# Performance work log

Hardware: AMD Instinct MI355X
Metric: run time of the kernel (lower is better)

The kernel has to match this reference:

```python
import jax, jax.numpy as jnp
import numpy as np

N = 100_000      # nodes
E = 2_500_000    # edges (nnz), avg degree 25
D_IN = 32
D_OUT = 32


def setup_inputs() -> dict:
    key = jax.random.key(0)
    k1, k2, k3, k4 = jax.random.split(key, 4)
    X = jax.random.normal(k1, (N, D_IN), dtype=jnp.float32)
    # CSR row offsets: sorted, anchored at 0 and E
    rp = jnp.sort(jax.random.randint(k2, (N + 1,), 0, E, dtype=jnp.int32))
    rp = rp.at[0].set(0).at[-1].set(E)
    ci = jax.random.randint(k3, (E,), 0, N, dtype=jnp.int32)
    W = (jax.random.normal(k4, (D_IN, D_OUT), dtype=jnp.float32)
         * (1.0 / np.sqrt(D_OUT)).astype(np.float32))
    dummy = jnp.zeros((1,), dtype=jnp.int32)
    return {
        "X": X,
        "weights": W,
        "row_pointers": rp,
        "column_index": ci,
        "blockPartition": dummy,
        "edgeToColumn": dummy,
        "edgeToRow": dummy,
        "hybrid_type": dummy,
        "row_nzr": dummy,
        "col_nzr": dummy,
    }


def reference(X, weights, row_pointers, column_index, blockPartition,
              edgeToColumn, edgeToRow, hybrid_type, row_nzr, col_nzr):
    # Fused GIN: X_prime = A @ X (CSR neighbor sum), then X_prime @ W.
    # Recover per-edge destination row from CSR offsets: row r owns edges
    # in [row_pointers[r], row_pointers[r+1]).
    edge_ids = jnp.arange(E, dtype=row_pointers.dtype)
    row = jnp.searchsorted(row_pointers, edge_ids, side="right") - 1  # [E]
    gathered = X[column_index]                       # [E, D_IN] (irregular gather)
    X_prime = jax.ops.segment_sum(gathered, row, num_segments=N)  # [N, D_IN]
    return X_prime @ weights                          # [N, D_OUT]
```

## Files before the change

kernel.cpp:

```cpp
#include <hip/hip_runtime.h>

#define D 32

__global__ __launch_bounds__(256, 8)
void xw_kernel(const float* __restrict__ X, const float* __restrict__ W,
               float* __restrict__ Y, int n) {
    const int lane = threadIdx.x & 63;
    const int j    = lane & 31;
    const int wid  = blockIdx.x * (blockDim.x >> 6) + (threadIdx.x >> 6);
    const int nw   = gridDim.x * (blockDim.x >> 6);

    float w[D];
    #pragma unroll
    for (int d = 0; d < D; ++d) w[d] = W[d * D + j];

    for (int r = wid; r <= n; r += nw) {
        float o0 = 0.f, o1 = 0.f;
        if (r < n) {
            const float* xr =
                X + (size_t)(unsigned)__builtin_amdgcn_readfirstlane(r) * D;
            #pragma unroll
            for (int d = 0; d < D; d += 2) {
                o0 = fmaf(xr[d],     w[d],     o0);
                o1 = fmaf(xr[d + 1], w[d + 1], o1);
            }
        }
        if (lane < 32) Y[(size_t)r * D + j] = o0 + o1;
    }
}

template <int K>
__device__ __forceinline__ void gather_acc(const float* __restrict__ Y,
                                           int myci, int base, int g, int s,
                                           float4& acc) {
    float4 x[K];
    #pragma unroll
    for (int it = 0; it < K; ++it) {
        int c = __shfl(myci, (base + it) * 8 + g, 64);
        x[it] = ((const float4*)(Y + (size_t)(unsigned)c * D))[s];
    }
    #pragma unroll
    for (int it = 0; it < K; ++it) {
        acc.x += x[it].x; acc.y += x[it].y;
        acc.z += x[it].z; acc.w += x[it].w;
    }
}

__device__ __forceinline__ void ladder(const float* __restrict__ Y, int myci,
                                       int nv, int g, int s, float4& acc) {
    switch ((nv + 7) >> 3) {
        case 1: gather_acc<1>(Y, myci, 0, g, s, acc); break;
        case 2: gather_acc<2>(Y, myci, 0, g, s, acc); break;
        case 3: gather_acc<3>(Y, myci, 0, g, s, acc); break;
        case 4: gather_acc<4>(Y, myci, 0, g, s, acc); break;
        case 5: gather_acc<4>(Y, myci, 0, g, s, acc);
                gather_acc<1>(Y, myci, 4, g, s, acc); break;
        case 6: gather_acc<4>(Y, myci, 0, g, s, acc);
                gather_acc<2>(Y, myci, 4, g, s, acc); break;
        case 7: gather_acc<4>(Y, myci, 0, g, s, acc);
                gather_acc<3>(Y, myci, 4, g, s, acc); break;
        default: gather_acc<4>(Y, myci, 0, g, s, acc);
                 gather_acc<4>(Y, myci, 4, g, s, acc); break;
    }
}

__global__ __launch_bounds__(256, 8)
void agg_kernel(const float* __restrict__ Y, const int* __restrict__ rp,
                const int* __restrict__ ci, float* __restrict__ out, int n) {
    const int lane = threadIdx.x & 63;
    const int g  = lane >> 3;
    const int s  = lane & 7;
    const int zr = n;

    const int wid = (blockIdx.x * blockDim.x + threadIdx.x) >> 6;
    const int nw  = (gridDim.x * blockDim.x) >> 6;

    int r = __builtin_amdgcn_readfirstlane(wid);
    if (r >= n) return;

    int start = rp[r];
    int end   = rp[r + 1];
    {
        int nv0 = end - start; nv0 = nv0 > 64 ? 64 : nv0;
        start = start;
    }
    int nv0 = end - start; nv0 = nv0 > 64 ? 64 : nv0;
    int myci = (lane < nv0) ? ci[start + lane] : zr;

    while (true) {
        const int deg = end - start;
        const int rn  = r + nw;
        const bool has_next = rn < n;

        int nstart = 0, nend = 0, next_ci = zr;
        if (has_next) {
            nstart = rp[rn];
            nend   = rp[rn + 1];
            int nnv = nend - nstart; nnv = nnv > 64 ? 64 : nnv;
            next_ci = (lane < nnv) ? ci[nstart + lane] : zr;
        }

        float4 acc = make_float4(0.f, 0.f, 0.f, 0.f);
        if (deg > 0) {
            int nv = deg > 64 ? 64 : deg;
            ladder(Y, myci, nv, g, s, acc);
            for (int cb = 64; cb < deg; cb += 64) {
                int rem = deg - cb;
                int nv2 = rem > 64 ? 64 : rem;
                int c2  = (lane < nv2) ? ci[start + cb + lane] : zr;
                ladder(Y, c2, nv2, g, s, acc);
            }
        }

        #pragma unroll
        for (int off = 8; off < 64; off <<= 1) {
            acc.x += __shfl_xor(acc.x, off, 64);
            acc.y += __shfl_xor(acc.y, off, 64);
            acc.z += __shfl_xor(acc.z, off, 64);
            acc.w += __shfl_xor(acc.w, off, 64);
        }
        if (lane < 8) ((float4*)(out + (size_t)r * D))[s] = acc;

        if (!has_next) break;
        r = rn; start = nstart; end = nend; myci = next_ci;
    }
}

__global__ __launch_bounds__(256, 4)
void gin_fused(const float* __restrict__ X,
               const float* __restrict__ W,
               const int* __restrict__ rp,
               const int* __restrict__ ci,
               float* __restrict__ out,
               int n) {
    __shared__ float Wl[D * D];

    int tid = threadIdx.x;
    {
        const float4* Wv = (const float4*)W;
        float4* Wlv = (float4*)Wl;
        Wlv[tid] = Wv[tid];
    }
    __syncthreads();

    int wave = tid >> 6;
    int lane = tid & 63;
    int row = blockIdx.x * 4 + wave;
    if (row >= n) return;

    int start = rp[row];
    int deg   = rp[row + 1] - start;

    int g = lane >> 3;
    int s = lane & 7;

    float4 acc = make_float4(0.f, 0.f, 0.f, 0.f);

    for (int cb = 0; cb < deg; cb += 64) {
        int rem = deg - cb;
        int nv  = rem < 64 ? rem : 64;
        int myci = (lane < nv) ? ci[start + cb + lane] : 0;
        {
            float4 x[4]; float m[4];
            #pragma unroll
            for (int it = 0; it < 4; ++it) {
                int l = it * 8 + g;
                int c = __shfl(myci, l, 64);
                m[it] = (l < rem) ? 1.f : 0.f;
                x[it] = ((const float4*)(X + (size_t)c * D))[s];
            }
            #pragma unroll
            for (int it = 0; it < 4; ++it) {
                acc.x = fmaf(m[it], x[it].x, acc.x);
                acc.y = fmaf(m[it], x[it].y, acc.y);
                acc.z = fmaf(m[it], x[it].z, acc.z);
                acc.w = fmaf(m[it], x[it].w, acc.w);
            }
        }
        if (rem > 32) {
            float4 x[4]; float m[4];
            #pragma unroll
            for (int it = 0; it < 4; ++it) {
                int l = (it + 4) * 8 + g;
                int c = __shfl(myci, l, 64);
                m[it] = (l < rem) ? 1.f : 0.f;
                x[it] = ((const float4*)(X + (size_t)c * D))[s];
            }
            #pragma unroll
            for (int it = 0; it < 4; ++it) {
                acc.x = fmaf(m[it], x[it].x, acc.x);
                acc.y = fmaf(m[it], x[it].y, acc.y);
                acc.z = fmaf(m[it], x[it].z, acc.z);
                acc.w = fmaf(m[it], x[it].w, acc.w);
            }
        }
    }

    #pragma unroll
    for (int off = 8; off < 64; off <<= 1) {
        acc.x += __shfl_xor(acc.x, off, 64);
        acc.y += __shfl_xor(acc.y, off, 64);
        acc.z += __shfl_xor(acc.z, off, 64);
        acc.w += __shfl_xor(acc.w, off, 64);
    }

    int j = lane & 31;
    float o = 0.f;
    #pragma unroll
    for (int sg = 0; sg < 8; ++sg) {
        float ax = __shfl(acc.x, sg, 64);
        float ay = __shfl(acc.y, sg, 64);
        float az = __shfl(acc.z, sg, 64);
        float aw = __shfl(acc.w, sg, 64);
        int d = 4 * sg;
        o = fmaf(ax, Wl[(d    ) * D + j], o);
        o = fmaf(ay, Wl[(d + 1) * D + j], o);
        o = fmaf(az, Wl[(d + 2) * D + j], o);
        o = fmaf(aw, Wl[(d + 3) * D + j], o);
    }
    if (lane < 32) out[(size_t)row * D + j] = o;
}

extern "C" void kernel_launch(void* const* d_in, const int* in_sizes, int n_in,
                              void* d_out, int out_size, void* d_ws, size_t ws_size,
                              hipStream_t stream) {
    const float* X  = (const float*)d_in[0];
    const float* W  = (const float*)d_in[1];
    const int*   rp = (const int*)d_in[2];
    const int*   ci = (const int*)d_in[3];
    float* out = (float*)d_out;

    int n = in_sizes[2] - 1;
    size_t ybytes = (size_t)(n + 1) * D * sizeof(float);

    if (ws_size >= ybytes) {
        float* Y = (float*)d_ws;
        hipLaunchKernelGGL(xw_kernel, dim3(1024), dim3(256), 0, stream,
                           X, W, Y, n);
        int nwaves = (n + 3) / 4;
        int blocks = nwaves < 2048 ? nwaves : 2048;
        hipLaunchKernelGGL(agg_kernel, dim3(blocks), dim3(256), 0, stream,
                           Y, rp, ci, out, n);
    } else {
        hipLaunchKernelGGL(gin_fused, dim3((n + 3) / 4), dim3(256), 0, stream,
                           X, W, rp, ci, out, n);
    }
}
```

Before: 132.9 us.

## Store intermediate XW in fp16 and gather 16 edges per pass

The intermediate Y = X·W is now written as fp16, which halves the bytes the random neighbour gather in the aggregation kernel must fetch. Each lane now loads 8 halves, so 16 edges are handled per pass and the shuffle reduction and output store are reshaped to match. The xw kernel also processes two rows per wave using float4 loads, and its grid is doubled. The cost is reduced precision in the intermediate values, which may push results past the accuracy tolerance.

```diff
diff --git a/kernel.cpp b/kernel.cpp
--- a/kernel.cpp
+++ b/kernel.cpp
@@ -1,75 +1,74 @@
 #include <hip/hip_runtime.h>
 
 #define D 32
+
+typedef _Float16 half8 __attribute__((ext_vector_type(8)));
 
 __global__ __launch_bounds__(256, 8)
 void xw_kernel(const float* __restrict__ X, const float* __restrict__ W,
-               float* __restrict__ Y, int n) {
+               _Float16* __restrict__ Y16, int n) {
     const int lane = threadIdx.x & 63;
     const int j    = lane & 31;
-    const int wid  = blockIdx.x * (blockDim.x >> 6) + (threadIdx.x >> 6);
-    const int nw   = gridDim.x * (blockDim.x >> 6);
+    const int h    = lane >> 5;
+    const int wid  = (blockIdx.x * blockDim.x + threadIdx.x) >> 6;
+    const int nw   = (gridDim.x * blockDim.x) >> 6;
 
     float w[D];
     #pragma unroll
     for (int d = 0; d < D; ++d) w[d] = W[d * D + j];
 
-    for (int r = wid; r <= n; r += nw) {
-        float o0 = 0.f, o1 = 0.f;
+    for (int r0 = 2 * wid; r0 <= n; r0 += 2 * nw) {
+        const int r = r0 + h;
+        float o = 0.f;
         if (r < n) {
-            const float* xr =
-                X + (size_t)(unsigned)__builtin_amdgcn_readfirstlane(r) * D;
-            #pragma unroll
-            for (int d = 0; d < D; d += 2) {
-                o0 = fmaf(xr[d],     w[d],     o0);
-                o1 = fmaf(xr[d + 1], w[d + 1], o1);
-            }
-        }
-        if (lane < 32) Y[(size_t)r * D + j] = o0 + o1;
+            const float4* xr = (const float4*)(X + (size_t)r * D);
+            #pragma unroll
+            for (int k = 0; k < 8; ++k) {
+                float4 xv = xr[k];
+                o = fmaf(xv.x, w[4 * k    ], o);
+                o = fmaf(xv.y, w[4 * k + 1], o);
+                o = fmaf(xv.z, w[4 * k + 2], o);
+                o = fmaf(xv.w, w[4 * k + 3], o);
+            }
+        }
+        if (r <= n) Y16[(size_t)r * D + j] = (_Float16)o;
     }
 }
 
 template <int K>
-__device__ __forceinline__ void gather_acc(const float* __restrict__ Y,
-                                           int myci, int base, int g, int s,
-                                           float4& acc) {
-    float4 x[K];
+__device__ __forceinline__ void gather16(const _Float16* __restrict__ Y16,
+                                         int myci, int base, int g, int s,
+                                         float* acc) {
+    half8 x[K];
     #pragma unroll
     for (int it = 0; it < K; ++it) {
-        int c = __shfl(myci, (base + it) * 8 + g, 64);
-        x[it] = ((const float4*)(Y + (size_t)(unsigned)c * D))[s];
+        int c = __shfl(myci, (base + it) * 16 + g, 64);
+        x[it] = ((const half8*)(Y16 + (size_t)(unsigned)c * D))[s];
     }
     #pragma unroll
     for (int it = 0; it < K; ++it) {
-        acc.x += x[it].x; acc.y += x[it].y;
-        acc.z += x[it].z; acc.w += x[it].w;
-    }
-}
-
-__device__ __forceinline__ void ladder(const float* __restrict__ Y, int myci,
-                                       int nv, int g, int s, float4& acc) {
-    switch ((nv + 7) >> 3) {
-        case 1: gather_acc<1>(Y, myci, 0, g, s, acc); break;
-        case 2: gather_acc<2>(Y, myci, 0, g, s, acc); break;
-        case 3: gather_acc<3>(Y, myci, 0, g, s, acc); break;
-        case 4: gather_acc<4>(Y, myci, 0, g, s, acc); break;
-        case 5: gather_acc<4>(Y, myci, 0, g, s, acc);
-                gather_acc<1>(Y, myci, 4, g, s, acc); break;
-        case 6: gather_acc<4>(Y, myci, 0, g, s, acc);
-                gather_acc<2>(Y, myci, 4, g, s, acc); break;
-        case 7: gather_acc<4>(Y, myci, 0, g, s, acc);
-                gather_acc<3>(Y, myci, 4, g, s, acc); break;
-        default: gather_acc<4>(Y, myci, 0, g, s, acc);
-                 gather_acc<4>(Y, myci, 4, g, s, acc); break;
+        #pragma unroll
+        for (int e = 0; e < 8; ++e) acc[e] += (float)x[it][e];
+    }
+}
+
+__device__ __forceinline__ void ladder16(const _Float16* __restrict__ Y16,
+                                         int myci, int nv, int g, int s,
+                                         float* acc) {
+    switch ((nv + 15) >> 4) {
+        case 1:  gather16<1>(Y16, myci, 0, g, s, acc); break;
+        case 2:  gather16<2>(Y16, myci, 0, g, s, acc); break;
+        case 3:  gather16<3>(Y16, myci, 0, g, s, acc); break;
+        default: gather16<4>(Y16, myci, 0, g, s, acc); break;
     }
 }
 
 __global__ __launch_bounds__(256, 8)
-void agg_kernel(const float* __restrict__ Y, const int* __restrict__ rp,
+void agg_kernel(const _Float16* __restrict__ Y16, const int* __restrict__ rp,
                 const int* __restrict__ ci, float* __restrict__ out, int n) {
     const int lane = threadIdx.x & 63;
-    const int g  = lane >> 3;
-    const int s  = lane & 7;
+    const int g  = lane >> 2;
+    const int s  = lane & 3;
     const int zr = n;
 
     const int wid = (blockIdx.x * blockDim.x + threadIdx.x) >> 6;
@@ -80,12 +79,8 @@
 
     int start = rp[r];
     int end   = rp[r + 1];
-    {
-        int nv0 = end - start; nv0 = nv0 > 64 ? 64 : nv0;
-        start = start;
-    }
-    int nv0 = end - start; nv0 = nv0 > 64 ? 64 : nv0;
-    int myci = (lane < nv0) ? ci[start + lane] : zr;
+    int nv0   = end - start; nv0 = nv0 > 64 ? 64 : nv0;
+    int myci  = (lane < nv0) ? ci[start + lane] : zr;
 
     while (true) {
         const int deg = end - start;
@@ -100,26 +95,28 @@
             next_ci = (lane < nnv) ? ci[nstart + lane] : zr;
         }
 
-        float4 acc = make_float4(0.f, 0.f, 0.f, 0.f);
+        float acc[8] = {0.f, 0.f, 0.f, 0.f, 0.f, 0.f, 0.f, 0.f};
         if (deg > 0) {
             int nv = deg > 64 ? 64 : deg;
-            ladder(Y, myci, nv, g, s, acc);
+            ladder16(Y16, myci, nv, g, s, acc);
             for (int cb = 64; cb < deg; cb += 64) {
                 int rem = deg - cb;
                 int nv2 = rem > 64 ? 64 : rem;
                 int c2  = (lane < nv2) ? ci[start + cb + lane] : zr;
-                ladder(Y, c2, nv2, g, s, acc);
+                ladder16(Y16, c2, nv2, g, s, acc);
             }
         }
 
         #pragma unroll
-        for (int off = 8; off < 64; off <<= 1) {
-            acc.x += __shfl_xor(acc.x, off, 64);
-            acc.y += __shfl_xor(acc.y, off, 64);
-            acc.z += __shfl_xor(acc.z, off, 64);
-            acc.w += __shfl_xor(acc.w, off, 64);
-        }
-        if (lane < 8) ((float4*)(out + (size_t)r * D))[s] = acc;
+        for (int off = 4; off < 64; off <<= 1) {
+            #pragma unroll
+            for (int e = 0; e < 8; ++e) acc[e] += __shfl_xor(acc[e], off, 64);
+        }
+        if (lane < 4) {
+            float4* op = (float4*)(out + (size_t)r * D + s * 8);
+            op[0] = make_float4(acc[0], acc[1], acc[2], acc[3]);
+            op[1] = make_float4(acc[4], acc[5], acc[6], acc[7]);
+        }
 
         if (!has_next) break;
         r = rn; start = nstart; end = nend; myci = next_ci;
@@ -231,16 +228,16 @@
     float* out = (float*)d_out;
 
     int n = in_sizes[2] - 1;
-    size_t ybytes = (size_t)(n + 1) * D * sizeof(float);
+    size_t ybytes = (size_t)(n + 1) * D * sizeof(_Float16);
 
     if (ws_size >= ybytes) {
-        float* Y = (float*)d_ws;
-        hipLaunchKernelGGL(xw_kernel, dim3(1024), dim3(256), 0, stream,
-                           X, W, Y, n);
+        _Float16* Y16 = (_Float16*)d_ws;
+        hipLaunchKernelGGL(xw_kernel, dim3(2048), dim3(256), 0, stream,
+                           X, W, Y16, n);
         int nwaves = (n + 3) / 4;
         int blocks = nwaves < 2048 ? nwaves : 2048;
         hipLaunchKernelGGL(agg_kernel, dim3(blocks), dim3(256), 0, stream,
-                           Y, rp, ci, out, n);
+                           Y16, rp, ci, out, n);
     } else {
         hipLaunchKernelGGL(gin_fused, dim3((n + 3) / 4), dim3(256), 0, stream,
                            X, W, rp, ci, out, n);
```

Result: slower. 139.9 us (+5.3%).
